# Kernel tuning notes

Measured on AMD Instinct MI355X. Metric: run time of the kernel, lower is better.

## Reference

```python
import jax, jax.numpy as jnp
import numpy as np

LN_EPS = 1e-5

def layernorm(x, w, b, eps=LN_EPS):
    m = jnp.mean(x, -1, keepdims=True)
    v = jnp.mean(jnp.square(x - m), -1, keepdims=True)
    return (x - m) * jax.lax.rsqrt(v + eps) * w + b

def to_seq(x, k):
    # x: (B,d,H,W) -> (B,d,L) along scan direction k
    B, d, H, W = x.shape
    if k >= 2:
        x = jnp.swapaxes(x, 2, 3)  # column-major scan
    s = x.reshape(B, d, H * W)
    if k % 2 == 1:
        s = s[:, :, ::-1]  # reversed scan
    return s

def from_seq(y, k, H, W):
    B, d, L = y.shape
    if k % 2 == 1:
        y = y[:, :, ::-1]
    if k >= 2:
        y = jnp.swapaxes(y.reshape(B, d, W, H), 2, 3)
    else:
        y = y.reshape(B, d, H, W)
    return y

def ss2d(x, k, Win, cw, cb, Wx, Wdt, dtb, A_log, Dp, nw, nb, Wout):
    # x: (B,H,W,d) single-direction SS2D (VMamba-style selective scan)
    B, H, W, d = x.shape
    xz = x @ Win                                   # (B,H,W,2d)
    xin, z = jnp.split(xz, 2, axis=-1)
    xc = jnp.transpose(xin, (0, 3, 1, 2))          # (B,d,H,W)
    xc = jax.lax.conv_general_dilated(xc, cw, (1, 1), ((1, 1), (1, 1)),
                                      feature_group_count=d) + cb[None, :, None, None]
    xc = jax.nn.silu(xc)
    u = to_seq(xc, k)                              # (B,d,L)
    x_dbl = jnp.einsum('bdl,rd->brl', u, Wx)       # dt_rank + 2*N projections
    dtr = Wdt.shape[1]; N = A_log.shape[1]
    dt, Bm, Cm = jnp.split(x_dbl, [dtr, dtr + N], axis=1)
    delta = jax.nn.softplus(jnp.einsum('brl,dr->bdl', dt, Wdt) + dtb[None, :, None])
    A = -jnp.exp(A_log)                            # (d,N)
    dA = jnp.exp(delta[..., None] * A[None, :, None, :])                 # (B,d,L,N)
    dBu = (delta * u)[..., None] * jnp.transpose(Bm, (0, 2, 1))[:, None]  # (B,d,L,N)
    def comb(c1, c2):
        a1, b1 = c1; a2, b2 = c2
        return a1 * a2, a2 * b1 + b2
    _, h = jax.lax.associative_scan(comb, (dA, dBu), axis=2)  # parallel linear scan
    y = jnp.einsum('bdln,bnl->bdl', h, Cm) + Dp[:, None] * u
    y = jnp.transpose(from_seq(y, k, H, W), (0, 2, 3, 1))      # (B,H,W,d)
    y = layernorm(y, nw, nb)
    y = y * jax.nn.silu(z)
    return y @ Wout

def reference(x, norm_w, norm_b, fc1_w, fc1_b, fc2_w, fc2_b, Win, conv_w, conv_b,
              Wx, Wdt, dt_bias, A_log, Dp, onorm_w, onorm_b, Wout, proj_w, proj_b,
              skip_scale):
    B, C, H, W = x.shape
    xs = jnp.transpose(x.reshape(B, C, H * W), (0, 2, 1))  # (B,L,C)
    xs = layernorm(xs, norm_w, norm_b)
    z = jnp.mean(xs, axis=1)                               # squeeze: (B,C)
    se = jax.nn.sigmoid(jax.nn.relu(z @ fc1_w + fc1_b) @ fc2_w + fc2_b)
    xh = xs.reshape(B, H, W, C)
    d = C // 4
    outs = [ss2d(xh[..., k * d:(k + 1) * d], k, Win[k], conv_w[k], conv_b[k],
                 Wx[k], Wdt[k], dt_bias[k], A_log[k], Dp[k], onorm_w[k],
                 onorm_b[k], Wout[k]) for k in range(4)]
    xm = jnp.concatenate(outs, -1) * skip_scale * xh
    xm = xm.reshape(B, H * W, C) * se[:, None, :]
    xm = layernorm(xm, norm_w, norm_b)
    xm = xm @ proj_w + proj_b
    return jnp.transpose(xm, (0, 2, 1)).reshape(B, C, H, W)

def setup_inputs():
    key = jax.random.key(0)
    ks = jax.random.split(key, 12)
    B, C, H, W = 16, 512, 48, 48
    d, N, dtr, red = C // 4, 1, 8, C // 16
    def rn(k, shp, s=0.02):
        return (jax.random.normal(k, shp) * s).astype(jnp.float32)
    return {
        'x': jax.random.normal(ks[0], (B, C, H, W), jnp.float32),
        'norm_w': jnp.ones((C,), jnp.float32), 'norm_b': jnp.zeros((C,), jnp.float32),
        'fc1_w': rn(ks[1], (C, red)), 'fc1_b': jnp.zeros((red,), jnp.float32),
        'fc2_w': rn(ks[2], (red, C)), 'fc2_b': jnp.zeros((C,), jnp.float32),
        'Win': rn(ks[3], (4, d, 2 * d)),
        'conv_w': rn(ks[4], (4, d, 1, 3, 3), 0.1),
        'conv_b': jnp.zeros((4, d), jnp.float32),
        'Wx': rn(ks[5], (4, dtr + 2 * N, d)),
        'Wdt': rn(ks[6], (4, d, dtr), 0.1),
        'dt_bias': jnp.full((4, d), -4.6, jnp.float32),
        'A_log': jnp.zeros((4, d, N), jnp.float32),
        'Dp': jnp.ones((4, d), jnp.float32),
        'onorm_w': jnp.ones((4, d), jnp.float32), 'onorm_b': jnp.zeros((4, d), jnp.float32),
        'Wout': rn(ks[7], (4, d, d)),
        'proj_w': rn(ks[8], (C, C)), 'proj_b': jnp.zeros((C,), jnp.float32),
        'skip_scale': jnp.ones((1,), jnp.float32),
    }
```

## Files before the change

kernel.cpp:

```cpp
#include <hip/hip_runtime.h>
#include <math.h>

#define DEV static __device__ __forceinline__

typedef unsigned int  u32;
typedef unsigned short u16;

using bf16x8 = __attribute__((ext_vector_type(8))) __bf16;
using f32x4  = __attribute__((ext_vector_type(4))) float;

static constexpr int B_ = 16;
static constexpr int C_ = 512;
static constexpr int H_ = 48;
static constexpr int W_ = 48;
static constexpr int L_ = 2304;
static constexpr int M_ = B_ * L_;
static constexpr int SEG_ = 48;
static constexpr int TSEG_ = 48;
static constexpr int NLB_ = 144;

DEV float silu_(float v) { return v / (1.f + __expf(-v)); }
DEV float bflo(u32 p) { return __uint_as_float(p << 16); }
DEV float bfhi(u32 p) { return __uint_as_float(p & 0xffff0000u); }
DEV float bf2f(u16 v) { return __uint_as_float(((u32)v) << 16); }
DEV u16 f2bf(float f) { u32 u = __float_as_uint(f); u32 r = u + 0x7fffu + ((u >> 16) & 1u); return (u16)(r >> 16); }

DEV void seg_affine(int k, int s, int& sp0, int& step) {
  if (k == 0)      { sp0 = 48 * s;        step = 1;   }
  else if (k == 1) { sp0 = 2303 - 48 * s; step = -1;  }
  else if (k == 2) { sp0 = s;             step = 48;  }
  else             { sp0 = 2303 - s;      step = -48; }
}

DEV void stage_tile(u16* Ls, const u16* __restrict__ g, int ld) {
  const int tid = threadIdx.x;
  #pragma unroll
  for (int i = 0; i < 4; ++i) {
    int c = i * 256 + tid;
    int row = c >> 3, slot = c & 7;
    uint4 v = *(const uint4*)(g + (size_t)row * ld + slot * 8);
    int b = row * 128 + ((slot * 16) ^ ((row & 7) << 4));
    *(uint4*)((char*)Ls + b) = v;
  }
}

DEV bf16x8 lds_frag(const u16* Ls, int row, int kbyte) {
  int b = row * 128 + (kbyte ^ ((row & 7) << 4));
  return *(const bf16x8*)((const char*)Ls + b);
}

__global__ __launch_bounds__(256) void k_prep(const float* __restrict__ Win,
    const float* __restrict__ Wout, const float* __restrict__ projw,
    u16* __restrict__ WinT, u16* __restrict__ WoutT, u16* __restrict__ projwT) {
  int id = blockIdx.x * 256 + threadIdx.x;
  if (id < 131072) {
    int k = id >> 15, rem = id & 32767;
    int r = rem >> 8, n = rem & 255;
    WinT[(k << 15) + n * 128 + r] = f2bf(Win[id]);
  } else if (id < 196608) {
    int t = id - 131072;
    int k = t >> 14, rem = t & 16383;
    int r = rem >> 7, n = rem & 127;
    WoutT[(k << 14) + n * 128 + r] = f2bf(Wout[t]);
  } else {
    int t = id - 196608;
    int r = t >> 9, n = t & 511;
    projwT[n * 512 + r] = f2bf(projw[t]);
  }
}

__global__ __launch_bounds__(256) void k_ln_in(const float* __restrict__ x,
    const float* __restrict__ w, const float* __restrict__ bia, u16* __restrict__ xs,
    float* __restrict__ zpart) {
  __shared__ float tile[16 * 513];
  __shared__ float smean[16], srstd[16];
  const int b = blockIdx.y;
  const int l0 = blockIdx.x * 16;
  const int tid = threadIdx.x;
  const float* xb = x + (size_t)b * C_ * L_;
  for (int idx = tid; idx < C_ * 16; idx += 256) {
    int c = idx >> 4, lt = idx & 15;
    tile[lt * 513 + c] = xb[(size_t)c * L_ + l0 + lt];
  }
  __syncthreads();
  {
    const int j = tid & 15, g = tid >> 4;
    float s1 = 0.f, s2 = 0.f;
    #pragma unroll
    for (int i = 0; i < 32; ++i) {
      float v = tile[g * 513 + j + i * 16];
      s1 += v; s2 += v * v;
    }
    #pragma unroll
    for (int o = 8; o; o >>= 1) { s1 += __shfl_xor(s1, o, 16); s2 += __shfl_xor(s2, o, 16); }
    if (j == 0) {
      float mean = s1 * (1.f / C_);
      float var = s2 * (1.f / C_) - mean * mean;
      smean[g] = mean;
      srstd[g] = rsqrtf(var + 1e-5f);
    }
  }
  __syncthreads();
  float p0 = 0.f, p1 = 0.f;
  for (int idx = tid; idx < 16 * C_; idx += 256) {
    int lt = idx >> 9, c = idx & 511;
    float v = (tile[lt * 513 + c] - smean[lt]) * srstd[lt] * w[c] + bia[c];
    xs[((size_t)b * L_ + l0 + lt) * C_ + c] = f2bf(v);
    if (c == tid) p0 += v; else p1 += v;
  }
  float* zp = zpart + ((size_t)b * NLB_ + blockIdx.x) * 512;
  zp[tid] = p0;
  zp[tid + 256] = p1;
}

__global__ __launch_bounds__(256) void k_colsum_fin(const float* __restrict__ zpart, float* __restrict__ z) {
  const int c = blockIdx.x * 256 + threadIdx.x;
  const int b = blockIdx.y;
  float acc = 0.f;
  for (int s = 0; s < NLB_; ++s) acc += zpart[((size_t)b * NLB_ + s) * 512 + c];
  z[b * C_ + c] = acc * (1.f / L_);
}

__global__ __launch_bounds__(256) void k_se(const float* __restrict__ z,
    const float* __restrict__ fc1w, const float* __restrict__ fc1b,
    const float* __restrict__ fc2w, const float* __restrict__ fc2b, float* __restrict__ se) {
  __shared__ float zs[512];
  __shared__ float hs[32];
  const int b = blockIdx.x, tid = threadIdx.x;
  zs[tid] = z[b * C_ + tid];
  zs[tid + 256] = z[b * C_ + tid + 256];
  __syncthreads();
  if (tid < 32) {
    float a = fc1b[tid];
    for (int c = 0; c < 512; ++c) a += zs[c] * fc1w[c * 32 + tid];
    hs[tid] = fmaxf(a, 0.f);
  }
  __syncthreads();
  for (int c = tid; c < 512; c += 256) {
    float a = fc2b[c];
    #pragma unroll
    for (int r = 0; r < 32; ++r) a += hs[r] * fc2w[r * 512 + c];
    se[b * C_ + c] = 1.f / (1.f + __expf(-a));
  }
}

__global__ __launch_bounds__(256) void k_gemm_xz(const u16* __restrict__ xs,
    const u16* __restrict__ WinT, u16* __restrict__ xin, u16* __restrict__ zbuf) {
  __shared__ u16 lds[16384];
  u16* As = lds; u16* Bs = lds + 8192;
  const int k = blockIdx.z;
  const int nb = blockIdx.x;
  const int m0 = blockIdx.y * 128;
  const int tid = threadIdx.x, l = tid & 63, w = tid >> 6;
  const int wm = w >> 1, wn = w & 1;
  const int fr = l & 15, fg = l >> 4;
  f32x4 acc[4][4];
  #pragma unroll
  for (int mi = 0; mi < 4; ++mi)
    #pragma unroll
    for (int ni = 0; ni < 4; ++ni) acc[mi][ni] = (f32x4){0.f, 0.f, 0.f, 0.f};
  const u16* Ag = xs + (size_t)m0 * 512 + k * 128;
  const u16* Bg = WinT + (size_t)k * 32768 + (size_t)nb * 16384;
  #pragma unroll
  for (int kk0 = 0; kk0 < 128; kk0 += 64) {
    stage_tile(As, Ag + kk0, 512);
    stage_tile(Bs, Bg + kk0, 128);
    __syncthreads();
    bf16x8 af[2][4], bfr[2][4];
    #pragma unroll
    for (int h = 0; h < 2; ++h)
      #pragma unroll
      for (int s = 0; s < 4; ++s) {
        af[h][s]  = lds_frag(As, wm * 64 + s * 16 + fr, h * 64 + fg * 16);
        bfr[h][s] = lds_frag(Bs, wn * 64 + s * 16 + fr, h * 64 + fg * 16);
      }
    #pragma unroll
    for (int h = 0; h < 2; ++h)
      #pragma unroll
      for (int mi = 0; mi < 4; ++mi)
        #pragma unroll
        for (int ni = 0; ni < 4; ++ni)
          acc[mi][ni] = __builtin_amdgcn_mfma_f32_16x16x32_bf16(af[h][mi], bfr[h][ni], acc[mi][ni], 0, 0, 0);
    __syncthreads();
  }
  #pragma unroll
  for (int mi = 0; mi < 4; ++mi)
    #pragma unroll
    for (int ni = 0; ni < 4; ++ni)
      #pragma unroll
      for (int j = 0; j < 4; ++j)
        lds[(wm * 64 + mi * 16 + fg * 4 + j) * 128 + wn * 64 + ni * 16 + fr] = f2bf(acc[mi][ni][j]);
  __syncthreads();
  u16* dst = (nb == 0 ? xin : zbuf) + ((size_t)k * M_ + m0) * 128;
  for (int idx = tid; idx < 128 * 16; idx += 256) {
    int row = idx >> 4, q = idx & 15;
    *(uint4*)&dst[(size_t)row * 128 + q * 8] = *(const uint4*)&lds[row * 128 + q * 8];
  }
}

__global__ __launch_bounds__(256) void k_dwconv(const u16* __restrict__ xin,
    const float* __restrict__ cw, const float* __restrict__ cb, const float* __restrict__ Wx,
    u16* __restrict__ xc, float* __restrict__ xdbl) {
  __shared__ float taps[9 * 144];
  __shared__ float wxs[10 * 144];
  __shared__ float part[16 * 161];
  const int kb = blockIdx.y;
  const int k = kb >> 4;
  const int tid = threadIdx.x;
  for (int i = tid; i < 1152; i += 256) {
    int dc = i / 9, t = i - dc * 9;
    taps[t * 144 + (dc >> 3) * 9 + (dc & 7)] = cw[((size_t)k * 128 + dc) * 9 + t];
  }
  for (int i = tid; i < 1280; i += 256) {
    int r = i >> 7, dc = i & 127;
    wxs[r * 144 + (dc >> 3) * 9 + (dc & 7)] = Wx[(size_t)k * 1280 + i];
  }
  __syncthreads();
  const int sl = tid >> 4, g = tid & 15;
  const int sp = blockIdx.x * 16 + sl;
  const int h = sp / W_, w = sp % W_;
  const int dc0 = g * 8;
  const int tb = g * 9;
  float acc[8];
  {
    float4 b0 = *(const float4*)(cb + k * 128 + dc0);
    float4 b1 = *(const float4*)(cb + k * 128 + dc0 + 4);
    acc[0] = b0.x; acc[1] = b0.y; acc[2] = b0.z; acc[3] = b0.w;
    acc[4] = b1.x; acc[5] = b1.y; acc[6] = b1.z; acc[7] = b1.w;
  }
  const u16* base = xin + (size_t)kb * L_ * 128 + dc0;
  #pragma unroll
  for (int dy = -1; dy <= 1; ++dy) {
    int hh = h + dy;
    if (hh < 0 || hh >= H_) continue;
    #pragma unroll
    for (int dx = -1; dx <= 1; ++dx) {
      int ww = w + dx;
      if (ww < 0 || ww >= W_) continue;
      uint4 v = *(const uint4*)(base + (size_t)(hh * W_ + ww) * 128);
      const float* tp = &taps[((dy + 1) * 3 + dx + 1) * 144 + tb];
      acc[0] += tp[0] * bflo(v.x);
      acc[1] += tp[1] * bfhi(v.x);
      acc[2] += tp[2] * bflo(v.y);
      acc[3] += tp[3] * bfhi(v.y);
      acc[4] += tp[4] * bflo(v.z);
      acc[5] += tp[5] * bfhi(v.z);
      acc[6] += tp[6] * bflo(v.w);
      acc[7] += tp[7] * bfhi(v.w);
    }
  }
  float u[8];
  u16 ov[8];
  #pragma unroll
  for (int j = 0; j < 8; ++j) { u[j] = silu_(acc[j]); ov[j] = f2bf(u[j]); }
  *(uint4*)(xc + ((size_t)kb * L_ + sp) * 128 + dc0) = *(const uint4*)ov;
  #pragma unroll
  for (int r = 0; r < 10; ++r) {
    const float* wr = &wxs[r * 144 + tb];
    float pv = 0.f;
    #pragma unroll
    for (int j = 0; j < 8; ++j) pv += wr[j] * u[j];
    part[sl * 161 + g * 10 + r] = pv;
  }
  __syncthreads();
  if (tid < 160) {
    int sl2 = tid / 10, r = tid - sl2 * 10;
    float s = 0.f;
    #pragma unroll
    for (int g2 = 0; g2 < 16; ++g2) s += part[sl2 * 161 + g2 * 10 + r];
    xdbl[((size_t)kb * L_ + blockIdx.x * 16 + sl2) * 16 + r] = s;
  }
}

__global__ __launch_bounds__(256) void k_delta(const float* __restrict__ xdbl,
    const float* __restrict__ Wdt, const float* __restrict__ dtb, u16* __restrict__ delt) {
  __shared__ float xrow[16][8];
  const int kb = blockIdx.y;
  const int k = kb >> 4;
  const int tid = threadIdx.x;
  const int sp0 = blockIdx.x * 16;
  if (tid < 128) {
    int sl = tid >> 3, r = tid & 7;
    xrow[sl][r] = xdbl[((size_t)kb * L_ + sp0 + sl) * 16 + r];
  }
  const int dc = tid & 127, shalf = tid >> 7;
  const float4 w0 = *(const float4*)(Wdt + (size_t)k * 1024 + dc * 8);
  const float4 w1 = *(const float4*)(Wdt + (size_t)k * 1024 + dc * 8 + 4);
  const float db = dtb[k * 128 + dc];
  __syncthreads();
  u16* dst = delt + ((size_t)kb * L_ + sp0 + shalf * 8) * 128 + dc;
  #pragma unroll
  for (int i = 0; i < 8; ++i) {
    const float* r = xrow[shalf * 8 + i];
    float dt = db + w0.x * r[0] + w0.y * r[1] + w0.z * r[2] + w0.w * r[3]
                  + w1.x * r[4] + w1.y * r[5] + w1.z * r[6] + w1.w * r[7];
    float delta = (dt > 20.f) ? dt : __logf(1.f + __expf(dt));
    dst[(size_t)i * 128] = f2bf(delta);
  }
}

__global__ __launch_bounds__(256) void k_scan_passA(const u16* __restrict__ xc,
    const u16* __restrict__ delt, const float* __restrict__ xdbl,
    const float* __restrict__ Alog, float* __restrict__ segA, float* __restrict__ segB) {
  const int kb = blockIdx.y;
  const int k = kb >> 4;
  const int s = blockIdx.x * 2 + (threadIdx.x >> 7);
  const int dc = threadIdx.x & 127;
  const float Aa = -__expf(Alog[k * 128 + dc]);
  int sp0, step;
  seg_affine(k, s, sp0, step);
  const u16* up = xc + ((size_t)kb * L_ + sp0) * 128 + dc;
  const u16* dp = delt + ((size_t)kb * L_ + sp0) * 128 + dc;
  const float* xr = xdbl + ((size_t)kb * L_ + sp0) * 16 + 8;
  const int ustep = step * 128, xstep = step * 16;
  float a = 1.f, bacc = 0.f;
  #pragma unroll 4
  for (int i = 0; i < TSEG_; ++i) {
    float Bm = *xr;
    float u = bf2f(*up);
    float delta = bf2f(*dp);
    float dA = __expf(delta * Aa);
    a *= dA;
    bacc = dA * bacc + delta * u * Bm;
    up += ustep; dp += ustep; xr += xstep;
  }
  segA[((size_t)kb * SEG_ + s) * 128 + dc] = a;
  segB[((size_t)kb * SEG_ + s) * 128 + dc] = bacc;
}

__global__ __launch_bounds__(128) void k_scan_passB(const float* __restrict__ segA,
    const float* __restrict__ segB, float* __restrict__ hpre) {
  const int kb = blockIdx.x;
  const int dc = threadIdx.x;
  float h = 0.f;
  for (int s = 0; s < SEG_; ++s) {
    size_t o = ((size_t)kb * SEG_ + s) * 128 + dc;
    hpre[o] = h;
    h = segA[o] * h + segB[o];
  }
}

__global__ __launch_bounds__(256) void k_scan_passC(u16* __restrict__ xc,
    const u16* __restrict__ delt, const float* __restrict__ xdbl, const u16* __restrict__ zbuf,
    const float* __restrict__ Alog, const float* __restrict__ Dp, const float* __restrict__ hpre,
    const float* __restrict__ ow, const float* __restrict__ ob) {
  const int unit = blockIdx.x * 4 + (threadIdx.x >> 6);
  const int kb = unit / SEG_;
  const int s = unit - kb * SEG_;
  const int k = kb >> 4;
  const int lane = threadIdx.x & 63;
  const float Aa0 = -__expf(Alog[k * 128 + lane]);
  const float Aa1 = -__expf(Alog[k * 128 + lane + 64]);
  const float Dv0 = Dp[k * 128 + lane],      Dv1 = Dp[k * 128 + lane + 64];
  const float lw0 = ow[k * 128 + lane],      lw1 = ow[k * 128 + lane + 64];
  const float lb0 = ob[k * 128 + lane],      lb1 = ob[k * 128 + lane + 64];
  int sp0, step;
  seg_affine(k, s, sp0, step);
  size_t base = ((size_t)kb * L_ + sp0) * 128 + lane;
  u16* up = xc + base;
  const u16* dp = delt + base;
  const u16* zp = zbuf + base;
  const float* xr = xdbl + ((size_t)kb * L_ + sp0) * 16 + 8;
  const int ustep = step * 128, xstep = step * 16;
  float h0 = hpre[((size_t)kb * SEG_ + s) * 128 + lane];
  float h1 = hpre[((size_t)kb * SEG_ + s) * 128 + lane + 64];
  for (int i = 0; i < TSEG_; ++i) {
    float Bm = xr[0], Cm = xr[1];
    float u0 = bf2f(up[0]), u1 = bf2f(up[64]);
    float d0 = bf2f(dp[0]), d1 = bf2f(dp[64]);
    float z0 = bf2f(zp[0]), z1 = bf2f(zp[64]);
    float dA0 = __expf(d0 * Aa0), dA1 = __expf(d1 * Aa1);
    h0 = dA0 * h0 + d0 * u0 * Bm;
    h1 = dA1 * h1 + d1 * u1 * Bm;
    float y0 = h0 * Cm + Dv0 * u0;
    float y1 = h1 * Cm + Dv1 * u1;
    float s1 = y0 + y1, s2 = y0 * y0 + y1 * y1;
    #pragma unroll
    for (int o = 32; o; o >>= 1) { s1 += __shfl_xor(s1, o, 64); s2 += __shfl_xor(s2, o, 64); }
    float mean = s1 * (1.f / 128.f);
    float rstd = rsqrtf(s2 * (1.f / 128.f) - mean * mean + 1e-5f);
    up[0]  = f2bf(((y0 - mean) * rstd * lw0 + lb0) * silu_(z0));
    up[64] = f2bf(((y1 - mean) * rstd * lw1 + lb1) * silu_(z1));
    up += ustep; dp += ustep; zp += ustep; xr += xstep;
  }
}

__global__ __launch_bounds__(256) void k_gemm_wout(const u16* __restrict__ t,
    const u16* __restrict__ WoutT, const u16* __restrict__ xs, const float* __restrict__ se,
    const float* __restrict__ skip, u16* __restrict__ xm2) {
  __shared__ u16 lds[16384];
  u16* As = lds; u16* Bs = lds + 8192;
  const int k = blockIdx.z;
  const int m0 = blockIdx.y * 128;
  const int tid = threadIdx.x, l = tid & 63, w = tid >> 6;
  const int wm = w >> 1, wn = w & 1;
  const int fr = l & 15, fg = l >> 4;
  f32x4 acc[4][4];
  #pragma unroll
  for (int mi = 0; mi < 4; ++mi)
    #pragma unroll
    for (int ni = 0; ni < 4; ++ni) acc[mi][ni] = (f32x4){0.f, 0.f, 0.f, 0.f};
  const u16* Ag = t + ((size_t)k * M_ + m0) * 128;
  const u16* Bg = WoutT + (size_t)k * 16384;
  #pragma unroll
  for (int kk0 = 0; kk0 < 128; kk0 += 64) {
    stage_tile(As, Ag + kk0, 128);
    stage_tile(Bs, Bg + kk0, 128);
    __syncthreads();
    bf16x8 af[2][4], bfr[2][4];
    #pragma unroll
    for (int h = 0; h < 2; ++h)
      #pragma unroll
      for (int s = 0; s < 4; ++s) {
        af[h][s]  = lds_frag(As, wm * 64 + s * 16 + fr, h * 64 + fg * 16);
        bfr[h][s] = lds_frag(Bs, wn * 64 + s * 16 + fr, h * 64 + fg * 16);
      }
    #pragma unroll
    for (int h = 0; h < 2; ++h)
      #pragma unroll
      for (int mi = 0; mi < 4; ++mi)
        #pragma unroll
        for (int ni = 0; ni < 4; ++ni)
          acc[mi][ni] = __builtin_amdgcn_mfma_f32_16x16x32_bf16(af[h][mi], bfr[h][ni], acc[mi][ni], 0, 0, 0);
    __syncthreads();
  }
  #pragma unroll
  for (int mi = 0; mi < 4; ++mi)
    #pragma unroll
    for (int ni = 0; ni < 4; ++ni)
      #pragma unroll
      for (int j = 0; j < 4; ++j)
        lds[(wm * 64 + mi * 16 + fg * 4 + j) * 128 + wn * 64 + ni * 16 + fr] = f2bf(acc[mi][ni][j]);
  __syncthreads();
  const float sk = skip[0];
  const int b = m0 / L_;
  for (int idx = tid; idx < 128 * 16; idx += 256) {
    int row = idx >> 4, q = idx & 15;
    int m = m0 + row, c = k * 128 + q * 8;
    uint4 cv = *(const uint4*)&lds[row * 128 + q * 8];
    uint4 xv = *(const uint4*)&xs[(size_t)m * 512 + c];
    float4 s0 = *(const float4*)&se[b * 512 + c];
    float4 s1 = *(const float4*)&se[b * 512 + c + 4];
    float o[8];
    o[0] = bflo(cv.x) * sk * bflo(xv.x) * s0.x;
    o[1] = bfhi(cv.x) * sk * bfhi(xv.x) * s0.y;
    o[2] = bflo(cv.y) * sk * bflo(xv.y) * s0.z;
    o[3] = bfhi(cv.y) * sk * bfhi(xv.y) * s0.w;
    o[4] = bflo(cv.z) * sk * bflo(xv.z) * s1.x;
    o[5] = bfhi(cv.z) * sk * bfhi(xv.z) * s1.y;
    o[6] = bflo(cv.w) * sk * bflo(xv.w) * s1.z;
    o[7] = bfhi(cv.w) * sk * bfhi(xv.w) * s1.w;
    u16 ov[8];
    #pragma unroll
    for (int j = 0; j < 8; ++j) ov[j] = f2bf(o[j]);
    *(uint4*)&xm2[(size_t)m * 512 + c] = *(const uint4*)ov;
  }
}

__global__ __launch_bounds__(256) void k_ln_rows512(const u16* __restrict__ in,
    const float* __restrict__ w, const float* __restrict__ bia, u16* __restrict__ outp) {
  const int row = blockIdx.x * 4 + (threadIdx.x >> 6);
  const int lane = threadIdx.x & 63;
  const u16* r = in + (size_t)row * C_;
  float v[8];
  float s1 = 0.f, s2 = 0.f;
  #pragma unroll
  for (int i = 0; i < 8; ++i) { v[i] = bf2f(r[lane + i * 64]); s1 += v[i]; s2 += v[i] * v[i]; }
  #pragma unroll
  for (int o = 32; o; o >>= 1) { s1 += __shfl_xor(s1, o, 64); s2 += __shfl_xor(s2, o, 64); }
  float mean = s1 * (1.f / C_);
  float rstd = rsqrtf(s2 * (1.f / C_) - mean * mean + 1e-5f);
  #pragma unroll
  for (int i = 0; i < 8; ++i) {
    int c = lane + i * 64;
    outp[(size_t)row * C_ + c] = f2bf((v[i] - mean) * rstd * w[c] + bia[c]);
  }
}

__global__ __launch_bounds__(256) void k_gemm_proj(const u16* __restrict__ xln,
    const u16* __restrict__ projwT, const float* __restrict__ projb, float* __restrict__ outp) {
  __shared__ float ldsp[8448];
  u16* As = (u16*)ldsp; u16* Bs = As + 8192;
  const int n0 = blockIdx.x * 128;
  const int m0 = blockIdx.y * 128;
  const int tid = threadIdx.x, l = tid & 63, w = tid >> 6;
  const int wm = w >> 1, wn = w & 1;
  const int fr = l & 15, fg = l >> 4;
  f32x4 acc[4][4];
  #pragma unroll
  for (int mi = 0; mi < 4; ++mi)
    #pragma unroll
    for (int ni = 0; ni < 4; ++ni) acc[mi][ni] = (f32x4){0.f, 0.f, 0.f, 0.f};
  const u16* Ag = xln + (size_t)m0 * 512;
  const u16* Bg = projwT + (size_t)n0 * 512;
  for (int kk0 = 0; kk0 < 512; kk0 += 64) {
    stage_tile(As, Ag + kk0, 512);
    stage_tile(Bs, Bg + kk0, 512);
    __syncthreads();
    bf16x8 af[2][4], bfr[2][4];
    #pragma unroll
    for (int h = 0; h < 2; ++h)
      #pragma unroll
      for (int s = 0; s < 4; ++s) {
        af[h][s]  = lds_frag(As, wm * 64 + s * 16 + fr, h * 64 + fg * 16);
        bfr[h][s] = lds_frag(Bs, wn * 64 + s * 16 + fr, h * 64 + fg * 16);
      }
    #pragma unroll
    for (int h = 0; h < 2; ++h)
      #pragma unroll
      for (int mi = 0; mi < 4; ++mi)
        #pragma unroll
        for (int ni = 0; ni < 4; ++ni)
          acc[mi][ni] = __builtin_amdgcn_mfma_f32_16x16x32_bf16(af[h][mi], bfr[h][ni], acc[mi][ni], 0, 0, 0);
    __syncthreads();
  }
  const int b = m0 / L_, sp0 = m0 % L_;
  #pragma unroll
  for (int half = 0; half < 2; ++half) {
    if (wn == half) {
      #pragma unroll
      for (int ni = 0; ni < 4; ++ni) {
        int nl = ni * 16 + fr;
        float bias = projb[n0 + half * 64 + nl];
        #pragma unroll
        for (int mi = 0; mi < 4; ++mi)
          #pragma unroll
          for (int j = 0; j < 4; ++j)
            ldsp[nl * 132 + wm * 64 + mi * 16 + fg * 4 + j] = acc[mi][ni][j] + bias;
      }
    }
    __syncthreads();
    for (int idx = tid; idx < 64 * 32; idx += 256) {
      int n = idx >> 5, mq = idx & 31;
      float4 v = *(const float4*)&ldsp[n * 132 + mq * 4];
      *(float4*)&outp[((size_t)b * 512 + n0 + half * 64 + n) * L_ + sp0 + mq * 4] = v;
    }
    __syncthreads();
  }
}

extern "C" void kernel_launch(void* const* d_in, const int* in_sizes, int n_in,
                              void* d_out, int out_size, void* d_ws, size_t ws_size,
                              hipStream_t stream) {
  const float* x     = (const float*)d_in[0];
  const float* nw    = (const float*)d_in[1];
  const float* nb    = (const float*)d_in[2];
  const float* fc1w  = (const float*)d_in[3];
  const float* fc1b  = (const float*)d_in[4];
  const float* fc2w  = (const float*)d_in[5];
  const float* fc2b  = (const float*)d_in[6];
  const float* Win   = (const float*)d_in[7];
  const float* convw = (const float*)d_in[8];
  const float* convb = (const float*)d_in[9];
  const float* Wx    = (const float*)d_in[10];
  const float* Wdt   = (const float*)d_in[11];
  const float* dtb   = (const float*)d_in[12];
  const float* Alog  = (const float*)d_in[13];
  const float* Dp    = (const float*)d_in[14];
  const float* onw   = (const float*)d_in[15];
  const float* onb   = (const float*)d_in[16];
  const float* Wout  = (const float*)d_in[17];
  const float* projw = (const float*)d_in[18];
  const float* projb = (const float*)d_in[19];
  const float* skip  = (const float*)d_in[20];
  float* outp = (float*)d_out;

  const size_t BIGE = (size_t)4 * B_ * L_ * 128;
  char* p = (char*)d_ws;
  auto carve = [&](size_t bytes) { char* r = p; p += (bytes + 255) & ~(size_t)255; return r; };
  u16*   xs     = (u16*)  carve(BIGE * 2);
  u16*   big1   = (u16*)  carve(BIGE * 2);
  u16*   big2   = (u16*)  carve(BIGE * 2);
  u16*   big3   = (u16*)  carve(BIGE * 2);
  float* xdbl   = (float*)carve((size_t)2359296 * 4);
  float* segA   = (float*)carve((size_t)393216 * 4);
  float* segB   = (float*)carve((size_t)393216 * 4);
  float* hpre   = (float*)carve((size_t)393216 * 4);
  float* zpart  = (float*)carve((size_t)B_ * NLB_ * 512 * 4);
  float* z      = (float*)carve((size_t)8192 * 4);
  float* se     = (float*)carve((size_t)8192 * 4);
  u16*   WinT   = (u16*)  carve((size_t)131072 * 2);
  u16*   WoutT  = (u16*)  carve((size_t)65536 * 2);
  u16*   projwT = (u16*)  carve((size_t)262144 * 2);

  k_prep<<<1792, 256, 0, stream>>>(Win, Wout, projw, WinT, WoutT, projwT);
  k_ln_in<<<dim3(NLB_, B_), 256, 0, stream>>>(x, nw, nb, xs, zpart);
  k_colsum_fin<<<dim3(2, B_), 256, 0, stream>>>(zpart, z);
  k_se<<<B_, 256, 0, stream>>>(z, fc1w, fc1b, fc2w, fc2b, se);
  k_gemm_xz<<<dim3(2, M_ / 128, 4), 256, 0, stream>>>(xs, WinT, big1, big2);
  k_dwconv<<<dim3(L_ / 16, 64), 256, 0, stream>>>(big1, convw, convb, Wx, big3, xdbl);
  k_delta<<<dim3(L_ / 16, 64), 256, 0, stream>>>(xdbl, Wdt, dtb, big1);
  k_scan_passA<<<dim3(SEG_ / 2, 64), 256, 0, stream>>>(big3, big1, xdbl, Alog, segA, segB);
  k_scan_passB<<<64, 128, 0, stream>>>(segA, segB, hpre);
  k_scan_passC<<<SEG_ * 64 / 4, 256, 0, stream>>>(big3, big1, xdbl, big2, Alog, Dp, hpre, onw, onb);
  k_gemm_wout<<<dim3(1, M_ / 128, 4), 256, 0, stream>>>(big3, WoutT, xs, se, skip, big2);
  k_ln_rows512<<<M_ / 4, 256, 0, stream>>>(big2, nw, nb, big1);
  k_gemm_proj<<<dim3(4, M_ / 128), 256, 0, stream>>>(big1, projwT, projb, outp);
}
```

Baseline: 327.6 us.

## Fuse Wout GEMM epilogue with 512-channel LayerNorm in one kernel

Replaces the per-direction Wout GEMM and the separate row LayerNorm kernel with a single kernel. Each block handles 32 rows across all four directions, stages the full 512-wide rows in LDS, applies the skip/SE scaling, computes LayerNorm stats, and writes the normalized output. This removes the round trip of the intermediate xm2 tensor through global memory and one launch. In exchange it uses smaller M tiles (32 rows, so each block reloads the Wout weights for every direction), has fewer MFMAs per B-fragment load, and needs more LDS per block, which may lower occupancy.

```diff
diff --git a/kernel.cpp b/kernel.cpp
--- a/kernel.cpp
+++ b/kernel.cpp
@@ -42,6 +42,14 @@
     int b = row * 128 + ((slot * 16) ^ ((row & 7) << 4));
     *(uint4*)((char*)Ls + b) = v;
   }
+}
+
+DEV void stage_tile32(u16* Ls, const u16* __restrict__ g, int ld) {
+  const int c = threadIdx.x;
+  int row = c >> 3, slot = c & 7;
+  uint4 v = *(const uint4*)(g + (size_t)row * ld + slot * 8);
+  int b = row * 128 + ((slot * 16) ^ ((row & 7) << 4));
+  *(uint4*)((char*)Ls + b) = v;
 }
 
 DEV bf16x8 lds_frag(const u16* Ls, int row, int kbyte) {
@@ -385,95 +393,98 @@
   }
 }
 
-__global__ __launch_bounds__(256) void k_gemm_wout(const u16* __restrict__ t,
+__global__ __launch_bounds__(256) void k_wout_ln(const u16* __restrict__ t,
     const u16* __restrict__ WoutT, const u16* __restrict__ xs, const float* __restrict__ se,
-    const float* __restrict__ skip, u16* __restrict__ xm2) {
-  __shared__ u16 lds[16384];
-  u16* As = lds; u16* Bs = lds + 8192;
-  const int k = blockIdx.z;
-  const int m0 = blockIdx.y * 128;
+    const float* __restrict__ skip, const float* __restrict__ nw, const float* __restrict__ nb,
+    u16* __restrict__ xln) {
+  __shared__ u16 As[2048];
+  __shared__ u16 Bs[8192];
+  __shared__ u16 stage[32 * 520];
+  const int m0 = blockIdx.x * 32;
   const int tid = threadIdx.x, l = tid & 63, w = tid >> 6;
   const int wm = w >> 1, wn = w & 1;
   const int fr = l & 15, fg = l >> 4;
-  f32x4 acc[4][4];
-  #pragma unroll
-  for (int mi = 0; mi < 4; ++mi)
-    #pragma unroll
-    for (int ni = 0; ni < 4; ++ni) acc[mi][ni] = (f32x4){0.f, 0.f, 0.f, 0.f};
-  const u16* Ag = t + ((size_t)k * M_ + m0) * 128;
-  const u16* Bg = WoutT + (size_t)k * 16384;
-  #pragma unroll
-  for (int kk0 = 0; kk0 < 128; kk0 += 64) {
-    stage_tile(As, Ag + kk0, 128);
-    stage_tile(Bs, Bg + kk0, 128);
-    __syncthreads();
-    bf16x8 af[2][4], bfr[2][4];
-    #pragma unroll
-    for (int h = 0; h < 2; ++h)
-      #pragma unroll
-      for (int s = 0; s < 4; ++s) {
-        af[h][s]  = lds_frag(As, wm * 64 + s * 16 + fr, h * 64 + fg * 16);
-        bfr[h][s] = lds_frag(Bs, wn * 64 + s * 16 + fr, h * 64 + fg * 16);
+  for (int k = 0; k < 4; ++k) {
+    f32x4 acc[4];
+    #pragma unroll
+    for (int ni = 0; ni < 4; ++ni) acc[ni] = (f32x4){0.f, 0.f, 0.f, 0.f};
+    const u16* Ag = t + ((size_t)k * M_ + m0) * 128;
+    const u16* Bg = WoutT + (size_t)k * 16384;
+    #pragma unroll
+    for (int kk0 = 0; kk0 < 128; kk0 += 64) {
+      stage_tile32(As, Ag + kk0, 128);
+      stage_tile(Bs, Bg + kk0, 128);
+      __syncthreads();
+      bf16x8 af[2], bfr[2][4];
+      #pragma unroll
+      for (int h = 0; h < 2; ++h) {
+        af[h] = lds_frag(As, wm * 16 + fr, h * 64 + fg * 16);
+        #pragma unroll
+        for (int s = 0; s < 4; ++s)
+          bfr[h][s] = lds_frag(Bs, wn * 64 + s * 16 + fr, h * 64 + fg * 16);
       }
-    #pragma unroll
-    for (int h = 0; h < 2; ++h)
-      #pragma unroll
-      for (int mi = 0; mi < 4; ++mi)
+      #pragma unroll
+      for (int h = 0; h < 2; ++h)
         #pragma unroll
         for (int ni = 0; ni < 4; ++ni)
-          acc[mi][ni] = __builtin_amdgcn_mfma_f32_16x16x32_bf16(af[h][mi], bfr[h][ni], acc[mi][ni], 0, 0, 0);
-    __syncthreads();
-  }
-  #pragma unroll
-  for (int mi = 0; mi < 4; ++mi)
+          acc[ni] = __builtin_amdgcn_mfma_f32_16x16x32_bf16(af[h], bfr[h][ni], acc[ni], 0, 0, 0);
+      __syncthreads();
+    }
     #pragma unroll
     for (int ni = 0; ni < 4; ++ni)
       #pragma unroll
       for (int j = 0; j < 4; ++j)
-        lds[(wm * 64 + mi * 16 + fg * 4 + j) * 128 + wn * 64 + ni * 16 + fr] = f2bf(acc[mi][ni][j]);
-  __syncthreads();
+        stage[(wm * 16 + fg * 4 + j) * 520 + k * 128 + wn * 64 + ni * 16 + fr] = f2bf(acc[ni][j]);
+  }
+  __syncthreads();
+  const int row = tid >> 3, t7 = tid & 7;
+  const int m = m0 + row;
+  const int b = m / L_;
   const float sk = skip[0];
-  const int b = m0 / L_;
-  for (int idx = tid; idx < 128 * 16; idx += 256) {
-    int row = idx >> 4, q = idx & 15;
-    int m = m0 + row, c = k * 128 + q * 8;
-    uint4 cv = *(const uint4*)&lds[row * 128 + q * 8];
-    uint4 xv = *(const uint4*)&xs[(size_t)m * 512 + c];
-    float4 s0 = *(const float4*)&se[b * 512 + c];
-    float4 s1 = *(const float4*)&se[b * 512 + c + 4];
+  float s1 = 0.f, s2 = 0.f;
+  #pragma unroll
+  for (int i = 0; i < 8; ++i) {
+    int col = t7 * 8 + i * 64;
+    uint4 cv = *(const uint4*)&stage[row * 520 + col];
+    uint4 xv = *(const uint4*)&xs[(size_t)m * 512 + col];
+    float4 e0 = *(const float4*)&se[b * 512 + col];
+    float4 e1 = *(const float4*)&se[b * 512 + col + 4];
     float o[8];
-    o[0] = bflo(cv.x) * sk * bflo(xv.x) * s0.x;
-    o[1] = bfhi(cv.x) * sk * bfhi(xv.x) * s0.y;
-    o[2] = bflo(cv.y) * sk * bflo(xv.y) * s0.z;
-    o[3] = bfhi(cv.y) * sk * bfhi(xv.y) * s0.w;
-    o[4] = bflo(cv.z) * sk * bflo(xv.z) * s1.x;
-    o[5] = bfhi(cv.z) * sk * bfhi(xv.z) * s1.y;
-    o[6] = bflo(cv.w) * sk * bflo(xv.w) * s1.z;
-    o[7] = bfhi(cv.w) * sk * bfhi(xv.w) * s1.w;
+    o[0] = bflo(cv.x) * sk * bflo(xv.x) * e0.x;
+    o[1] = bfhi(cv.x) * sk * bfhi(xv.x) * e0.y;
+    o[2] = bflo(cv.y) * sk * bflo(xv.y) * e0.z;
+    o[3] = bfhi(cv.y) * sk * bfhi(xv.y) * e0.w;
+    o[4] = bflo(cv.z) * sk * bflo(xv.z) * e1.x;
+    o[5] = bfhi(cv.z) * sk * bfhi(xv.z) * e1.y;
+    o[6] = bflo(cv.w) * sk * bflo(xv.w) * e1.z;
+    o[7] = bfhi(cv.w) * sk * bfhi(xv.w) * e1.w;
     u16 ov[8];
     #pragma unroll
-    for (int j = 0; j < 8; ++j) ov[j] = f2bf(o[j]);
-    *(uint4*)&xm2[(size_t)m * 512 + c] = *(const uint4*)ov;
-  }
-}
-
-__global__ __launch_bounds__(256) void k_ln_rows512(const u16* __restrict__ in,
-    const float* __restrict__ w, const float* __restrict__ bia, u16* __restrict__ outp) {
-  const int row = blockIdx.x * 4 + (threadIdx.x >> 6);
-  const int lane = threadIdx.x & 63;
-  const u16* r = in + (size_t)row * C_;
-  float v[8];
-  float s1 = 0.f, s2 = 0.f;
-  #pragma unroll
-  for (int i = 0; i < 8; ++i) { v[i] = bf2f(r[lane + i * 64]); s1 += v[i]; s2 += v[i] * v[i]; }
-  #pragma unroll
-  for (int o = 32; o; o >>= 1) { s1 += __shfl_xor(s1, o, 64); s2 += __shfl_xor(s2, o, 64); }
+    for (int j = 0; j < 8; ++j) { s1 += o[j]; s2 += o[j] * o[j]; ov[j] = f2bf(o[j]); }
+    *(uint4*)&stage[row * 520 + col] = *(const uint4*)ov;
+  }
+  #pragma unroll
+  for (int o = 4; o; o >>= 1) { s1 += __shfl_xor(s1, o, 64); s2 += __shfl_xor(s2, o, 64); }
   float mean = s1 * (1.f / C_);
   float rstd = rsqrtf(s2 * (1.f / C_) - mean * mean + 1e-5f);
   #pragma unroll
   for (int i = 0; i < 8; ++i) {
-    int c = lane + i * 64;
-    outp[(size_t)row * C_ + c] = f2bf((v[i] - mean) * rstd * w[c] + bia[c]);
+    int col = t7 * 8 + i * 64;
+    uint4 cv = *(const uint4*)&stage[row * 520 + col];
+    float4 w0 = *(const float4*)&nw[col];
+    float4 w1 = *(const float4*)&nw[col + 4];
+    float4 b0 = *(const float4*)&nb[col];
+    float4 b1 = *(const float4*)&nb[col + 4];
+    u16 ov[8];
+    ov[0] = f2bf((bflo(cv.x) - mean) * rstd * w0.x + b0.x);
+    ov[1] = f2bf((bfhi(cv.x) - mean) * rstd * w0.y + b0.y);
+    ov[2] = f2bf((bflo(cv.y) - mean) * rstd * w0.z + b0.z);
+    ov[3] = f2bf((bfhi(cv.y) - mean) * rstd * w0.w + b0.w);
+    ov[4] = f2bf((bflo(cv.z) - mean) * rstd * w1.x + b1.x);
+    ov[5] = f2bf((bfhi(cv.z) - mean) * rstd * w1.y + b1.y);
+    ov[6] = f2bf((bflo(cv.w) - mean) * rstd * w1.z + b1.z);
+    ov[7] = f2bf((bfhi(cv.w) - mean) * rstd * w1.w + b1.w);
+    *(uint4*)&xln[(size_t)m * 512 + col] = *(const uint4*)ov;
   }
 }
 
@@ -593,7 +604,6 @@
   k_scan_passA<<<dim3(SEG_ / 2, 64), 256, 0, stream>>>(big3, big1, xdbl, Alog, segA, segB);
   k_scan_passB<<<64, 128, 0, stream>>>(segA, segB, hpre);
   k_scan_passC<<<SEG_ * 64 / 4, 256, 0, stream>>>(big3, big1, xdbl, big2, Alog, Dp, hpre, onw, onb);
-  k_gemm_wout<<<dim3(1, M_ / 128, 4), 256, 0, stream>>>(big3, WoutT, xs, se, skip, big2);
-  k_ln_rows512<<<M_ / 4, 256, 0, stream>>>(big2, nw, nb, big1);
+  k_wout_ln<<<M_ / 32, 256, 0, stream>>>(big3, WoutT, xs, se, skip, nw, nb, big1);
   k_gemm_proj<<<dim3(4, M_ / 128), 256, 0, stream>>>(big1, projwT, projb, outp);
 }
```

Result: faster. 315.5 us (-3.7%).
